# Performance work log

Measured on AMD Instinct MI355X. Metric: run time of the kernel, lower is better.

## Reference

```python
import jax, jax.numpy as jnp
import numpy as np

N, E, DIM_H, H = 50000, 400000, 128, 8
D = DIM_H // H  # 16


def _ln(x, g, b, eps=1e-5):
    mu = jnp.mean(x, axis=-1, keepdims=True)
    var = jnp.var(x, axis=-1, keepdims=True)
    return (x - mu) * jax.lax.rsqrt(var + eps) * g + b


def setup_inputs() -> dict:
    key = jax.random.key(0)
    ks = jax.random.split(key, 20)
    s = 1.0 / np.sqrt(DIM_H)
    lin = lambda k, i, o: jax.random.uniform(k, (i, o), jnp.float32, -s, s)
    inp = {
        "node_feature": jax.random.normal(ks[0], (N, DIM_H), jnp.float32),
        "edge_feature": jax.random.normal(ks[1], (E, DIM_H), jnp.float32),
        "Wq": lin(ks[2], DIM_H, DIM_H), "bq": jnp.zeros((DIM_H,), jnp.float32),
        "Wk": lin(ks[3], DIM_H, DIM_H), "bk": jnp.zeros((DIM_H,), jnp.float32),
        "Wv": lin(ks[4], DIM_H, DIM_H), "bv": jnp.zeros((DIM_H,), jnp.float32),
        "We": lin(ks[5], DIM_H, DIM_H), "be": jnp.zeros((DIM_H,), jnp.float32),
        "Wg": lin(ks[6], DIM_H, DIM_H), "bg": jnp.zeros((DIM_H,), jnp.float32),
        "Wo": lin(ks[7], DIM_H, DIM_H), "bo": jnp.zeros((DIM_H,), jnp.float32),
        "Woe": lin(ks[8], DIM_H, DIM_H), "boe": jnp.zeros((DIM_H,), jnp.float32),
        "ln1_g": jnp.ones((DIM_H,), jnp.float32), "ln1_b": jnp.zeros((DIM_H,), jnp.float32),
        "ln1e_g": jnp.ones((DIM_H,), jnp.float32), "ln1e_b": jnp.zeros((DIM_H,), jnp.float32),
        "ln2_g": jnp.ones((DIM_H,), jnp.float32), "ln2_b": jnp.zeros((DIM_H,), jnp.float32),
        "W1": lin(ks[9], DIM_H, 2 * DIM_H), "b1": jnp.zeros((2 * DIM_H,), jnp.float32),
        "W2": lin(ks[10], 2 * DIM_H, DIM_H) / np.sqrt(2.0), "b2": jnp.zeros((DIM_H,), jnp.float32),
        "edge_index": jax.random.randint(ks[11], (2, E), 0, N, jnp.int32),
    }
    return inp


def reference(node_feature, edge_feature, Wq, bq, Wk, bk, Wv, bv, We, be, Wg, bg,
              Wo, bo, Woe, boe, ln1_g, ln1_b, ln1e_g, ln1e_b, ln2_g, ln2_b,
              W1, b1, W2, b2, edge_index):
    x_in, e_in = node_feature, edge_feature
    src, dst = edge_index[0], edge_index[1]
    n = x_in.shape[0]

    x = _ln(x_in, ln1_g, ln1_b)
    e = _ln(e_in, ln1e_g, ln1e_b)

    # node projections -> [N, H, D]
    q = (x @ Wq + bq).reshape(n, H, D)
    k = (x @ Wk + bk).reshape(n, H, D)
    v = (x @ Wv + bv).reshape(n, H, D)
    # edge projections -> [E, H, D]
    ea = (e @ We + be).reshape(-1, H, D)
    eg = (e @ Wg + bg).reshape(-1, H, D)

    # gather along edges: [E, H, D]
    edge_q = q[dst]
    edge_k = k[src]
    edge_v = v[src] * jax.nn.sigmoid(eg)

    s_elt = edge_q * edge_k + ea                      # [E, H, D] (also edge output)
    scores = jnp.clip(jnp.sum(s_elt, axis=-1) / np.sqrt(D), -5.0, 5.0)  # [E, H]

    # scatter-softmax over destination nodes, per head
    m = jax.ops.segment_max(scores, dst, num_segments=n)      # [N, H]
    ex = jnp.exp(scores - m[dst])                             # [E, H]
    ssum = jax.ops.segment_sum(ex, dst, num_segments=n)       # [N, H]
    alpha = ex / ssum[dst]                                    # [E, H]

    # scatter-add aggregation
    out = jax.ops.segment_sum(alpha[..., None] * edge_v, dst, num_segments=n)  # [N, H, D]
    out = out.reshape(n, H * D)

    x_out = x_in + out @ Wo + bo
    e_out = e_in + s_elt.reshape(-1, H * D) @ Woe + boe

    # FFN ('Single') with pre-norm + residual
    h = _ln(x_out, ln2_g, ln2_b)
    x_out = x_out + jax.nn.relu(h @ W1 + b1) @ W2 + b2
    return x_out, e_out
```

## Files before the change

kernel.cpp:

```cpp
#include <hip/hip_runtime.h>

#define NN 50000
#define NE 400000
#define CAP 64
#define PACKN (7*16384 + 32768 + 32768)
#define PACKB ((PACKN + 255)/256)

typedef unsigned int u32;
typedef unsigned short u16;
typedef __attribute__((ext_vector_type(8))) short short8;
typedef __attribute__((ext_vector_type(4))) float f32x4;
typedef __attribute__((ext_vector_type(4))) unsigned int u32x4;

union FragU { uint4 u; short8 s; };
union Chunk { uint4 v[4]; u32 d[16]; };

__device__ __forceinline__ float bflo(u32 w){ union{u32 i; float f;} v; v.i = w<<16; return v.f; }
__device__ __forceinline__ float bfhi(u32 w){ union{u32 i; float f;} v; v.i = w & 0xffff0000u; return v.f; }
__device__ __forceinline__ u32 packbf(float a, float b){
  union{float f;u32 i;} x, y; x.f=a; y.f=b;
  u32 xi = x.i + (((x.i>>16)&1u) + 0x7fffu);
  u32 yi = y.i + (((y.i>>16)&1u) + 0x7fffu);
  return (xi>>16) | (yi & 0xffff0000u);
}

#define BAR() do { \
  asm volatile("s_waitcnt lgkmcnt(0)" ::: "memory"); \
  __builtin_amdgcn_s_barrier(); \
  asm volatile("" ::: "memory"); \
} while(0)

__device__ __forceinline__ int swz64(int row, int cp){ return row*64 + (cp ^ ((row&7)<<2)); }

__device__ __forceinline__ void stage_ln(const float* __restrict__ src, long base, long nrows,
                                         const float* __restrict__ gam, const float* __restrict__ bet,
                                         u32* __restrict__ tile, int t)
{
  int row = t>>2, sub = t&3;
  bool valid = (base + row) < nrows;
  const float* p = src + (base+row)*128 + sub*32;
  float4 x[8];
  float s=0.f, s2=0.f;
  #pragma unroll
  for(int q=0;q<8;++q){
    x[q] = valid ? *(const float4*)(p + 4*q) : make_float4(0.f,0.f,0.f,0.f);
    s  += x[q].x + x[q].y + x[q].z + x[q].w;
    s2 += x[q].x*x[q].x + x[q].y*x[q].y + x[q].z*x[q].z + x[q].w*x[q].w;
  }
  s  += __shfl_xor(s,1);  s  += __shfl_xor(s,2);
  s2 += __shfl_xor(s2,1); s2 += __shfl_xor(s2,2);
  float mu  = s*(1.f/128.f);
  float var = fmaxf(s2*(1.f/128.f) - mu*mu, 0.f);
  float rs  = rsqrtf(var + 1e-5f);
  const float* gp = gam + sub*32; const float* bp = bet + sub*32;
  #pragma unroll
  for(int m4=0;m4<4;++m4){
    float4 g0 = *(const float4*)(gp + 8*m4);
    float4 g1 = *(const float4*)(gp + 8*m4 + 4);
    float4 b0 = *(const float4*)(bp + 8*m4);
    float4 b1 = *(const float4*)(bp + 8*m4 + 4);
    float4 xa = x[2*m4], xb = x[2*m4+1];
    uint4 wv;
    wv.x = packbf((xa.x-mu)*rs*g0.x+b0.x, (xa.y-mu)*rs*g0.y+b0.y);
    wv.y = packbf((xa.z-mu)*rs*g0.z+b0.z, (xa.w-mu)*rs*g0.w+b0.w);
    wv.z = packbf((xb.x-mu)*rs*g1.x+b1.x, (xb.y-mu)*rs*g1.y+b1.y);
    wv.w = packbf((xb.z-mu)*rs*g1.z+b1.z, (xb.w-mu)*rs*g1.w+b1.w);
    *(uint4*)&tile[swz64(row, sub*16 + m4*4)] = wv;
  }
}

__device__ __forceinline__ void stage_ln8(const float* __restrict__ src, long base,
                                          const float* __restrict__ gam, const float* __restrict__ bet,
                                          u32* __restrict__ tile, int t)
{
  int row = t>>3, sub = t&7;
  const float* p = src + (base+row)*128 + sub*16;
  float4 x[4];
  float s=0.f, s2=0.f;
  #pragma unroll
  for(int q=0;q<4;++q){
    x[q] = *(const float4*)(p + 4*q);
    s  += x[q].x + x[q].y + x[q].z + x[q].w;
    s2 += x[q].x*x[q].x + x[q].y*x[q].y + x[q].z*x[q].z + x[q].w*x[q].w;
  }
  s  += __shfl_xor(s,1);  s  += __shfl_xor(s,2);  s  += __shfl_xor(s,4);
  s2 += __shfl_xor(s2,1); s2 += __shfl_xor(s2,2); s2 += __shfl_xor(s2,4);
  float mu  = s*(1.f/128.f);
  float var = fmaxf(s2*(1.f/128.f) - mu*mu, 0.f);
  float rs  = rsqrtf(var + 1e-5f);
  const float* gp = gam + sub*16; const float* bp = bet + sub*16;
  #pragma unroll
  for(int m4=0;m4<2;++m4){
    float4 g0 = *(const float4*)(gp + 8*m4);
    float4 g1 = *(const float4*)(gp + 8*m4 + 4);
    float4 b0 = *(const float4*)(bp + 8*m4);
    float4 b1 = *(const float4*)(bp + 8*m4 + 4);
    float4 xa = x[2*m4], xb = x[2*m4+1];
    uint4 wv;
    wv.x = packbf((xa.x-mu)*rs*g0.x+b0.x, (xa.y-mu)*rs*g0.y+b0.y);
    wv.y = packbf((xa.z-mu)*rs*g0.z+b0.z, (xa.w-mu)*rs*g0.w+b0.w);
    wv.z = packbf((xb.x-mu)*rs*g1.x+b1.x, (xb.y-mu)*rs*g1.y+b1.y);
    wv.w = packbf((xb.z-mu)*rs*g1.z+b1.z, (xb.w-mu)*rs*g1.w+b1.w);
    *(uint4*)&tile[swz64(row, sub*8 + m4*4)] = wv;
  }
}

__device__ __forceinline__ void gemmT8(const u16* __restrict__ PW, int NT, int mtoff,
                                       const u32* __restrict__ tile, int row, int l,
                                       f32x4 acc[8])
{
  int g = l>>4;
  #pragma unroll
  for(int kc=0;kc<4;++kc){
    FragU bf; bf.u = *(const uint4*)&tile[swz64(row, kc*16 + g*4)];
    #pragma unroll
    for(int mt=0;mt<8;++mt){
      FragU af; af.u = ((const uint4*)PW)[(size_t)(kc*NT + mtoff + mt)*64 + l];
      acc[mt] = __builtin_amdgcn_mfma_f32_16x16x32_bf16(af.s, bf.s, acc[mt], 0,0,0);
    }
  }
}

__device__ __forceinline__ void gemmT4(const u16* __restrict__ PW, int NT, int mtoff,
                                       const u32* __restrict__ tile, int row, int l,
                                       f32x4 acc[4])
{
  int g = l>>4;
  #pragma unroll
  for(int kc=0;kc<4;++kc){
    FragU bf; bf.u = *(const uint4*)&tile[swz64(row, kc*16 + g*4)];
    #pragma unroll
    for(int m=0;m<4;++m){
      FragU af; af.u = ((const uint4*)PW)[(size_t)(kc*NT + mtoff + m)*64 + l];
      acc[m] = __builtin_amdgcn_mfma_f32_16x16x32_bf16(af.s, bf.s, acc[m], 0,0,0);
    }
  }
}

__global__ __launch_bounds__(256)
void k_prep(const float* __restrict__ Wq, const float* __restrict__ Wk,
            const float* __restrict__ Wv, const float* __restrict__ We,
            const float* __restrict__ Wg, const float* __restrict__ Woe,
            const float* __restrict__ Wo, const float* __restrict__ W1,
            const float* __restrict__ W2, u16* __restrict__ dst,
            const int* __restrict__ eidx, int* __restrict__ cnt, int* __restrict__ elist)
{
  if (blockIdx.x < PACKB){
    int i = blockIdx.x*256 + threadIdx.x;
    const float* src; int N, idx;
    if (i < 7*16384){
      int m = i >> 14; idx = i & 16383; N=128;
      src = (m==0)?Wq:(m==1)?Wk:(m==2)?Wv:(m==3)?We:(m==4)?Wg:(m==5)?Woe:Wo;
    } else if (i < 7*16384 + 32768){ idx = i - 7*16384; N=256; src = W1; }
    else if (i < PACKN){ idx = i - 7*16384 - 32768; N=128; src = W2; }
    else return;
    int j = idx & 7, l = (idx>>3) & 63;
    int rest = idx >> 9;
    int NT = N >> 4;
    int nt = rest % NT, kc = rest / NT;
    int k = kc*32 + (l>>4)*8 + j;
    int n = nt*16 + (l&15);
    union{float f;u32 u;} x; x.f = src[(size_t)k*N + n];
    dst[i] = (u16)((x.u + (((x.u>>16)&1u) + 0x7fffu)) >> 16);
  } else {
    int e = (blockIdx.x - PACKB)*256 + threadIdx.x;
    if (e < NE){
      int d = eidx[NE+e];
      int pos = atomicAdd(&cnt[d], 1);
      if (pos < CAP) elist[(size_t)d*CAP + pos] = e;
    }
  }
}

__global__ __launch_bounds__(256)
void k_qkv(const float* __restrict__ xin,
           const float* __restrict__ l1g, const float* __restrict__ l1b,
           const u16* __restrict__ pWq, const float* __restrict__ bq,
           const u16* __restrict__ pWk, const float* __restrict__ bk,
           const u16* __restrict__ pWv, const float* __restrict__ bv,
           u32* __restrict__ qv, u32* __restrict__ kv, u32* __restrict__ vv)
{
  __shared__ u32 tile[64*64];
  int t = threadIdx.x;
  long base = (long)blockIdx.x * 64;
  stage_ln(xin, base, NN, l1g, l1b, tile, t);
  BAR();
  int w = t>>6, l = t&63, g = l>>4;
  int row = w*16 + (l&15);
  long node = base + row;
  bool valid = node < NN;

  f32x4 acc[8];
  const u16* pws[3] = {pWq, pWk, pWv};
  const float* bbs[3] = {bq, bk, bv};
  u32* outs[3] = {qv, kv, vv};
  #pragma unroll
  for(int s3=0;s3<3;++s3){
    #pragma unroll
    for(int mt=0;mt<8;++mt) acc[mt] = (f32x4){0.f,0.f,0.f,0.f};
    gemmT8(pws[s3], 8, 0, tile, row, l, acc);
    if (valid){
      Chunk c;
      #pragma unroll
      for(int mt=0;mt<8;++mt){
        float4 bb = *(const float4*)(bbs[s3] + mt*16 + g*4);
        c.d[mt*2]   = packbf(acc[mt][0]+bb.x, acc[mt][1]+bb.y);
        c.d[mt*2+1] = packbf(acc[mt][2]+bb.z, acc[mt][3]+bb.w);
      }
      uint4* op = (uint4*)(outs[s3] + node*64 + g*16);
      #pragma unroll
      for(int i=0;i<4;++i) op[i] = c.v[i];
    }
  }
}

__global__ __launch_bounds__(512)
void k_edge(const float* __restrict__ ein,
            const float* __restrict__ l1eg, const float* __restrict__ l1eb,
            const u16* __restrict__ pWg, const float* __restrict__ bg,
            const u16* __restrict__ pWe, const float* __restrict__ be,
            const u16* __restrict__ pWoe, const float* __restrict__ boe,
            const int* __restrict__ eidx,
            const u32* __restrict__ qv, const u32* __restrict__ kv, const u32* __restrict__ vv,
            u32* __restrict__ gvp, float* __restrict__ escp,
            float* __restrict__ eout)
{
  __shared__ u32 tile[64*64];
  int t = threadIdx.x;
  long base = (long)blockIdx.x * 64;
  stage_ln8(ein, base, l1eg, l1eb, tile, t);

  int w = t>>6, l = t&63, g = l>>4;
  int rg = w&3, half = w>>2;
  int row = rg*16 + (l&15);
  long edge = base + row;
  int s_ = eidx[edge], d_ = eidx[NE + edge];
  BAR();

  float4 er[4];
  #pragma unroll
  for(int m=0;m<4;++m)
    er[m] = *(const float4*)(ein + edge*128 + (half*4+m)*16 + g*4);

  const uint4* qp = (const uint4*)(qv + (size_t)d_*64 + g*16 + half*8);
  const uint4* kp = (const uint4*)(kv + (size_t)s_*64 + g*16 + half*8);
  uint4 qa = qp[0], qb = qp[1];
  uint4 ka = kp[0], kb = kp[1];
  uint2 qw[4] = {{qa.x,qa.y},{qa.z,qa.w},{qb.x,qb.y},{qb.z,qb.w}};
  uint2 kw[4] = {{ka.x,ka.y},{ka.z,ka.w},{kb.x,kb.y},{kb.z,kb.w}};

  f32x4 acc[4];
  #pragma unroll
  for(int m=0;m<4;++m) acc[m] = (f32x4){0.f,0.f,0.f,0.f};
  gemmT4(pWe, 8, half*4, tile, row, l, acc);
  float esc4[4];
  #pragma unroll
  for(int m=0;m<4;++m){
    int mt = half*4 + m;
    float4 bb = *(const float4*)(be + mt*16 + g*4);
    acc[m][0] += bb.x + bflo(qw[m].x)*bflo(kw[m].x);
    acc[m][1] += bb.y + bfhi(qw[m].x)*bfhi(kw[m].x);
    acc[m][2] += bb.z + bflo(qw[m].y)*bflo(kw[m].y);
    acc[m][3] += bb.w + bfhi(qw[m].y)*bfhi(kw[m].y);
    float ps = acc[m][0]+acc[m][1]+acc[m][2]+acc[m][3];
    ps += __shfl_xor(ps, 16);
    ps += __shfl_xor(ps, 32);
    float sc = fminf(fmaxf(ps*0.25f, -5.f), 5.f);
    esc4[m] = __expf(sc);
  }
  if (g==0){
    f32x4 e0 = {esc4[0],esc4[1],esc4[2],esc4[3]};
    __builtin_nontemporal_store(e0, (f32x4*)(escp + (size_t)edge*8 + half*4));
  }
  const uint4* vp = (const uint4*)(vv + (size_t)s_*64 + g*16 + half*8);
  uint4 va = vp[0], vb = vp[1];
  uint2 vw[4] = {{va.x,va.y},{va.z,va.w},{vb.x,vb.y},{vb.z,vb.w}};

  f32x4 gac[4];
  #pragma unroll
  for(int m=0;m<4;++m) gac[m] = (f32x4){0.f,0.f,0.f,0.f};
  gemmT4(pWg, 8, half*4, tile, row, l, gac);
  {
    u32 gd[8];
    #pragma unroll
    for(int m=0;m<4;++m){
      int mt = half*4 + m;
      float4 bb = *(const float4*)(bg + mt*16 + g*4);
      float g0 = 1.f/(1.f+__expf(-(gac[m][0]+bb.x)));
      float g1 = 1.f/(1.f+__expf(-(gac[m][1]+bb.y)));
      float g2 = 1.f/(1.f+__expf(-(gac[m][2]+bb.z)));
      float g3 = 1.f/(1.f+__expf(-(gac[m][3]+bb.w)));
      gd[m*2]   = packbf(g0*bflo(vw[m].x), g1*bfhi(vw[m].x));
      gd[m*2+1] = packbf(g2*bflo(vw[m].y), g3*bfhi(vw[m].y));
    }
    u32x4* gp = (u32x4*)(gvp + (size_t)edge*64 + g*16 + half*8);
    u32x4 g0 = {gd[0],gd[1],gd[2],gd[3]};
    u32x4 g1 = {gd[4],gd[5],gd[6],gd[7]};
    __builtin_nontemporal_store(g0, gp);
    __builtin_nontemporal_store(g1, gp+1);
  }
  BAR();
  #pragma unroll
  for(int m=0;m<4;++m){
    int mt = half*4 + m;
    uint2 o;
    o.x = packbf(acc[m][0], acc[m][1]);
    o.y = packbf(acc[m][2], acc[m][3]);
    *(uint2*)&tile[swz64(row, mt*8 + g*2)] = o;
  }
  BAR();
  f32x4 oac[4];
  #pragma unroll
  for(int m=0;m<4;++m) oac[m] = (f32x4){0.f,0.f,0.f,0.f};
  gemmT4(pWoe, 8, half*4, tile, row, l, oac);
  #pragma unroll
  for(int m=0;m<4;++m){
    int mt = half*4 + m;
    float4 bb = *(const float4*)(boe + mt*16 + g*4);
    f32x4 o;
    o[0] = er[m].x + oac[m][0] + bb.x;
    o[1] = er[m].y + oac[m][1] + bb.y;
    o[2] = er[m].z + oac[m][2] + bb.z;
    o[3] = er[m].w + oac[m][3] + bb.w;
    __builtin_nontemporal_store(o, (f32x4*)(eout + edge*128 + mt*16 + g*4));
  }
}

__global__ __launch_bounds__(256)
void k_agg(const u32* __restrict__ gvp, const float* __restrict__ escp,
           const int* __restrict__ elist, const int* __restrict__ cnt,
           u32* __restrict__ xattnb)
{
  int w = threadIdx.x>>6, l = threadIdx.x&63;
  long n = (long)blockIdx.x*4 + w;
  if (n >= NN) return;
  int h = (l&15)>>1;
  int e = min(cnt[n], CAP);
  const int* el = elist + (size_t)n*CAP;
  float s0=0.f, s1=0.f, den=0.f;
  int i = 0;
  for (; i+8<=e; i+=8){
    int ed[8];
    #pragma unroll
    for(int j=0;j<8;++j) ed[j] = el[i+j];
    u32 gw[8]; float a[8];
    #pragma unroll
    for(int j=0;j<8;++j){ gw[j] = gvp[(size_t)ed[j]*64 + l]; a[j] = escp[(size_t)ed[j]*8 + h]; }
    #pragma unroll
    for(int j=0;j<8;++j){ s0 += a[j]*bflo(gw[j]); s1 += a[j]*bfhi(gw[j]); den += a[j]; }
  }
  if (i < e){
    int m = e - i;
    int ed[7]; u32 gw[7]; float a[7];
    #pragma unroll
    for(int j=0;j<7;++j) if (j < m) ed[j] = el[i+j];
    #pragma unroll
    for(int j=0;j<7;++j) if (j < m){ gw[j] = gvp[(size_t)ed[j]*64 + l]; a[j] = escp[(size_t)ed[j]*8 + h]; }
    #pragma unroll
    for(int j=0;j<7;++j) if (j < m){ s0 += a[j]*bflo(gw[j]); s1 += a[j]*bfhi(gw[j]); den += a[j]; }
  }
  float inv = den>0.f ? 1.f/den : 0.f;
  xattnb[n*64 + l] = packbf(s0*inv, s1*inv);
}

__global__ __launch_bounds__(256)
void k_out(const float* __restrict__ xin,
           const u32* __restrict__ xattnb,
           const u16* __restrict__ pWo, const float* __restrict__ bo,
           const float* __restrict__ l2g, const float* __restrict__ l2b,
           const u16* __restrict__ pW1, const float* __restrict__ b1p,
           const u16* __restrict__ pW2, const float* __restrict__ b2p,
           float* __restrict__ xout)
{
  __shared__ u32 tile[64*64];
  __shared__ u32 hhalf[64*64];
  int t = threadIdx.x;
  long base = (long)blockIdx.x * 64;
  {
    int row = t>>2, sub = t&3;
    long node = base + row;
    bool valid = node < NN;
    Chunk c;
    if (valid){
      const uint4* p = (const uint4*)(xattnb + node*64 + sub*16);
      #pragma unroll
      for(int i=0;i<4;++i) c.v[i] = p[i];
    } else {
      #pragma unroll
      for(int i=0;i<16;++i) c.d[i] = 0;
    }
    #pragma unroll
    for(int mt=0;mt<8;++mt){
      uint2 o; o.x = c.d[mt*2]; o.y = c.d[mt*2+1];
      *(uint2*)&tile[swz64(row, mt*8 + sub*2)] = o;
    }
  }
  BAR();
  int w = t>>6, l = t&63, g = l>>4;
  int row = w*16 + (l&15);
  long node = base + row;
  bool valid = node < NN;

  float4 xr[8];
  #pragma unroll
  for(int mt=0;mt<8;++mt)
    xr[mt] = valid ? *(const float4*)(xin + node*128 + mt*16 + g*4) : make_float4(0.f,0.f,0.f,0.f);

  f32x4 acc[8], xm[8];
  #pragma unroll
  for(int mt=0;mt<8;++mt) acc[mt] = (f32x4){0.f,0.f,0.f,0.f};
  gemmT8(pWo, 8, 0, tile, row, l, acc);
  #pragma unroll
  for(int mt=0;mt<8;++mt){
    float4 bb = *(const float4*)(bo + mt*16 + g*4);
    xm[mt][0] = xr[mt].x + acc[mt][0] + bb.x;
    xm[mt][1] = xr[mt].y + acc[mt][1] + bb.y;
    xm[mt][2] = xr[mt].z + acc[mt][2] + bb.z;
    xm[mt][3] = xr[mt].w + acc[mt][3] + bb.w;
  }
  float s=0.f, s2=0.f;
  #pragma unroll
  for(int mt=0;mt<8;++mt){
    s  += xm[mt][0]+xm[mt][1]+xm[mt][2]+xm[mt][3];
    s2 += xm[mt][0]*xm[mt][0]+xm[mt][1]*xm[mt][1]+xm[mt][2]*xm[mt][2]+xm[mt][3]*xm[mt][3];
  }
  s  += __shfl_xor(s,16);  s  += __shfl_xor(s,32);
  s2 += __shfl_xor(s2,16); s2 += __shfl_xor(s2,32);
  float mu  = s*(1.f/128.f);
  float var = fmaxf(s2*(1.f/128.f) - mu*mu, 0.f);
  float rs  = rsqrtf(var + 1e-5f);
  BAR();
  #pragma unroll
  for(int mt=0;mt<8;++mt){
    float4 gg = *(const float4*)(l2g + mt*16 + g*4);
    float4 bb = *(const float4*)(l2b + mt*16 + g*4);
    float h0 = (xm[mt][0]-mu)*rs*gg.x + bb.x;
    float h1 = (xm[mt][1]-mu)*rs*gg.y + bb.y;
    float h2 = (xm[mt][2]-mu)*rs*gg.z + bb.z;
    float h3 = (xm[mt][3]-mu)*rs*gg.w + bb.w;
    uint2 o; o.x = packbf(h0,h1); o.y = packbf(h2,h3);
    *(uint2*)&tile[swz64(row, mt*8 + g*2)] = o;
  }
  BAR();
  f32x4 oacc[8];
  #pragma unroll
  for(int mt=0;mt<8;++mt) oacc[mt] = (f32x4){0.f,0.f,0.f,0.f};
  #pragma unroll
  for(int hf=0; hf<2; ++hf){
    f32x4 dh[8];
    #pragma unroll
    for(int mt=0;mt<8;++mt) dh[mt] = (f32x4){0.f,0.f,0.f,0.f};
    gemmT8(pW1, 16, hf*8, tile, row, l, dh);
    #pragma unroll
    for(int mt=0;mt<8;++mt){
      int feat = hf*128 + mt*16 + g*4;
      float4 bb = *(const float4*)(b1p + feat);
      float h0 = fmaxf(dh[mt][0]+bb.x, 0.f);
      float h1 = fmaxf(dh[mt][1]+bb.y, 0.f);
      float h2 = fmaxf(dh[mt][2]+bb.z, 0.f);
      float h3 = fmaxf(dh[mt][3]+bb.w, 0.f);
      uint2 o; o.x = packbf(h0,h1); o.y = packbf(h2,h3);
      *(uint2*)&hhalf[swz64(row, mt*8 + g*2)] = o;
    }
    BAR();
    gemmT8(pW2 + (size_t)hf*16384, 8, 0, hhalf, row, l, oacc);
    BAR();
  }
  if (valid){
    #pragma unroll
    for(int mt=0;mt<8;++mt){
      float4 bb = *(const float4*)(b2p + mt*16 + g*4);
      f32x4 o;
      o[0] = xm[mt][0] + oacc[mt][0] + bb.x;
      o[1] = xm[mt][1] + oacc[mt][1] + bb.y;
      o[2] = xm[mt][2] + oacc[mt][2] + bb.z;
      o[3] = xm[mt][3] + oacc[mt][3] + bb.w;
      __builtin_nontemporal_store(o, (f32x4*)(xout + node*128 + mt*16 + g*4));
    }
  }
}

extern "C" void kernel_launch(void* const* d_in, const int* in_sizes, int n_in,
                              void* d_out, int out_size, void* d_ws, size_t ws_size,
                              hipStream_t stream) {
  (void)in_sizes; (void)n_in; (void)out_size; (void)ws_size;
  const float* xin = (const float*)d_in[0];
  const float* ein = (const float*)d_in[1];
  const float* Wq = (const float*)d_in[2];  const float* bq = (const float*)d_in[3];
  const float* Wk = (const float*)d_in[4];  const float* bk = (const float*)d_in[5];
  const float* Wv = (const float*)d_in[6];  const float* bv = (const float*)d_in[7];
  const float* We = (const float*)d_in[8];  const float* be = (const float*)d_in[9];
  const float* Wg = (const float*)d_in[10]; const float* bg = (const float*)d_in[11];
  const float* Wo = (const float*)d_in[12]; const float* bo = (const float*)d_in[13];
  const float* Woe= (const float*)d_in[14]; const float* boe= (const float*)d_in[15];
  const float* l1g= (const float*)d_in[16]; const float* l1b= (const float*)d_in[17];
  const float* l1eg=(const float*)d_in[18]; const float* l1eb=(const float*)d_in[19];
  const float* l2g= (const float*)d_in[20]; const float* l2b= (const float*)d_in[21];
  const float* W1 = (const float*)d_in[22]; const float* b1 = (const float*)d_in[23];
  const float* W2 = (const float*)d_in[24]; const float* b2 = (const float*)d_in[25];
  const int* eidx = (const int*)d_in[26];

  float* xout = (float*)d_out;
  float* eout = xout + (size_t)NN*128;

  float* escp = (float*)d_ws;
  u32* gvp = (u32*)(escp + (size_t)NE*8);
  u32* qv = gvp + (size_t)NE*64;
  u32* kv = qv + (size_t)NN*64;
  u32* vv = kv + (size_t)NN*64;
  u32* xattnb = vv + (size_t)NN*64;
  int* cnt = (int*)(xattnb + (size_t)NN*64);
  int* elist = cnt + NN;
  u16* pw  = (u16*)(elist + (size_t)NN*CAP);
  u16* pWq = pw;            u16* pWk = pWq + 16384;  u16* pWv = pWk + 16384;
  u16* pWe = pWv + 16384;   u16* pWg = pWe + 16384;  u16* pWoe= pWg + 16384;
  u16* pWo = pWoe + 16384;  u16* pW1 = pWo + 16384;  u16* pW2 = pW1 + 32768;

  hipMemsetAsync(cnt, 0, NN*sizeof(int), stream);
  k_prep<<<PACKB + (NE+255)/256, 256, 0, stream>>>(Wq,Wk,Wv,We,Wg,Woe,Wo,W1,W2, pw,
                                                   eidx, cnt, elist);

  k_qkv<<<(NN+63)/64, 256, 0, stream>>>(xin, l1g, l1b, pWq, bq, pWk, bk, pWv, bv, qv, kv, vv);
  k_edge<<<NE/64, 512, 0, stream>>>(ein, l1eg, l1eb, pWg, bg, pWe, be, pWoe, boe,
                                    eidx, qv, kv, vv, gvp, escp, eout);
  k_agg<<<(NN+3)/4, 256, 0, stream>>>(gvp, escp, elist, cnt, xattnb);
  k_out<<<(NN+63)/64, 256, 0, stream>>>(xin, xattnb, pWo, bo, l2g, l2b,
                                        pW1, b1, pW2, b2, xout);
}
```

Baseline: 421.5 us.

## Fuse We and Wg edge GEMMs into one interleaved packed weight pass

Packs an interleaved We/Wg weight matrix in k_prep so the edge kernel runs one 8-tile GEMM over the LDS tile instead of two separate 4-tile GEMMs, and hoists the V gather load earlier. The gated-value output layout changes, so k_agg's head index mapping and k_out's tile scatter are adjusted to match. This is meant to cut repeated A-fragment LDS reads and loop overhead, at the cost of more live accumulator registers in a 512-thread kernel. The escp store also switches from nontemporal to a plain store.

```diff
diff --git a/kernel.cpp b/kernel.cpp
--- a/kernel.cpp
+++ b/kernel.cpp
@@ -4,7 +4,8 @@
 #define NE 400000
 #define CAP 64
 #define PACKN (7*16384 + 32768 + 32768)
-#define PACKB ((PACKN + 255)/256)
+#define PACKN2 (PACKN + 32768)
+#define PACKB ((PACKN2 + 255)/256)
 
 typedef unsigned int u32;
 typedef unsigned short u16;
@@ -147,17 +148,26 @@
 {
   if (blockIdx.x < PACKB){
     int i = blockIdx.x*256 + threadIdx.x;
-    const float* src; int N, idx;
+    const float* src; int N, idx, nt_override = -1;
     if (i < 7*16384){
       int m = i >> 14; idx = i & 16383; N=128;
       src = (m==0)?Wq:(m==1)?Wk:(m==2)?Wv:(m==3)?We:(m==4)?Wg:(m==5)?Woe:Wo;
     } else if (i < 7*16384 + 32768){ idx = i - 7*16384; N=256; src = W1; }
     else if (i < PACKN){ idx = i - 7*16384 - 32768; N=128; src = W2; }
+    else if (i < PACKN2){
+      idx = i - PACKN; N=128;
+      int rest = idx >> 9;
+      int T = rest & 15;
+      int half = T>>3, within = T&7;
+      nt_override = half*4 + (within&3);
+      src = (within>>2) ? Wg : We;
+    }
     else return;
     int j = idx & 7, l = (idx>>3) & 63;
     int rest = idx >> 9;
-    int NT = N >> 4;
-    int nt = rest % NT, kc = rest / NT;
+    int NT = (nt_override >= 0) ? 16 : (N >> 4);
+    int nt = (nt_override >= 0) ? nt_override : (rest % NT);
+    int kc = rest / NT;
     int k = kc*32 + (l>>4)*8 + j;
     int n = nt*16 + (l&15);
     union{float f;u32 u;} x; x.f = src[(size_t)k*N + n];
@@ -217,8 +227,8 @@
 __global__ __launch_bounds__(512)
 void k_edge(const float* __restrict__ ein,
             const float* __restrict__ l1eg, const float* __restrict__ l1eb,
-            const u16* __restrict__ pWg, const float* __restrict__ bg,
-            const u16* __restrict__ pWe, const float* __restrict__ be,
+            const u16* __restrict__ pWeg, const float* __restrict__ bg,
+            const float* __restrict__ be,
             const u16* __restrict__ pWoe, const float* __restrict__ boe,
             const int* __restrict__ eidx,
             const u32* __restrict__ qv, const u32* __restrict__ kv, const u32* __restrict__ vv,
@@ -241,71 +251,66 @@
   #pragma unroll
   for(int m=0;m<4;++m)
     er[m] = *(const float4*)(ein + edge*128 + (half*4+m)*16 + g*4);
-
   const uint4* qp = (const uint4*)(qv + (size_t)d_*64 + g*16 + half*8);
   const uint4* kp = (const uint4*)(kv + (size_t)s_*64 + g*16 + half*8);
+  const uint4* vp = (const uint4*)(vv + (size_t)s_*64 + g*16 + half*8);
   uint4 qa = qp[0], qb = qp[1];
   uint4 ka = kp[0], kb = kp[1];
+  uint4 va = vp[0], vb = vp[1];
   uint2 qw[4] = {{qa.x,qa.y},{qa.z,qa.w},{qb.x,qb.y},{qb.z,qb.w}};
   uint2 kw[4] = {{ka.x,ka.y},{ka.z,ka.w},{kb.x,kb.y},{kb.z,kb.w}};
-
-  f32x4 acc[4];
-  #pragma unroll
-  for(int m=0;m<4;++m) acc[m] = (f32x4){0.f,0.f,0.f,0.f};
-  gemmT4(pWe, 8, half*4, tile, row, l, acc);
+  uint2 vw[4] = {{va.x,va.y},{va.z,va.w},{vb.x,vb.y},{vb.z,vb.w}};
+
+  f32x4 acc8[8];
+  #pragma unroll
+  for(int m=0;m<8;++m) acc8[m] = (f32x4){0.f,0.f,0.f,0.f};
+  gemmT8(pWeg, 16, half*8, tile, row, l, acc8);
+
   float esc4[4];
   #pragma unroll
   for(int m=0;m<4;++m){
     int mt = half*4 + m;
     float4 bb = *(const float4*)(be + mt*16 + g*4);
-    acc[m][0] += bb.x + bflo(qw[m].x)*bflo(kw[m].x);
-    acc[m][1] += bb.y + bfhi(qw[m].x)*bfhi(kw[m].x);
-    acc[m][2] += bb.z + bflo(qw[m].y)*bflo(kw[m].y);
-    acc[m][3] += bb.w + bfhi(qw[m].y)*bfhi(kw[m].y);
-    float ps = acc[m][0]+acc[m][1]+acc[m][2]+acc[m][3];
+    acc8[m][0] += bb.x + bflo(qw[m].x)*bflo(kw[m].x);
+    acc8[m][1] += bb.y + bfhi(qw[m].x)*bfhi(kw[m].x);
+    acc8[m][2] += bb.z + bflo(qw[m].y)*bflo(kw[m].y);
+    acc8[m][3] += bb.w + bfhi(qw[m].y)*bfhi(kw[m].y);
+    float ps = acc8[m][0]+acc8[m][1]+acc8[m][2]+acc8[m][3];
     ps += __shfl_xor(ps, 16);
     ps += __shfl_xor(ps, 32);
     float sc = fminf(fmaxf(ps*0.25f, -5.f), 5.f);
     esc4[m] = __expf(sc);
   }
   if (g==0){
-    f32x4 e0 = {esc4[0],esc4[1],esc4[2],esc4[3]};
-    __builtin_nontemporal_store(e0, (f32x4*)(escp + (size_t)edge*8 + half*4));
-  }
-  const uint4* vp = (const uint4*)(vv + (size_t)s_*64 + g*16 + half*8);
-  uint4 va = vp[0], vb = vp[1];
-  uint2 vw[4] = {{va.x,va.y},{va.z,va.w},{vb.x,vb.y},{vb.z,vb.w}};
-
-  f32x4 gac[4];
-  #pragma unroll
-  for(int m=0;m<4;++m) gac[m] = (f32x4){0.f,0.f,0.f,0.f};
-  gemmT4(pWg, 8, half*4, tile, row, l, gac);
+    float4 e0 = {esc4[0],esc4[1],esc4[2],esc4[3]};
+    *(float4*)(escp + (size_t)edge*8 + half*4) = e0;
+  }
   {
     u32 gd[8];
     #pragma unroll
     for(int m=0;m<4;++m){
       int mt = half*4 + m;
       float4 bb = *(const float4*)(bg + mt*16 + g*4);
-      float g0 = 1.f/(1.f+__expf(-(gac[m][0]+bb.x)));
-      float g1 = 1.f/(1.f+__expf(-(gac[m][1]+bb.y)));
-      float g2 = 1.f/(1.f+__expf(-(gac[m][2]+bb.z)));
-      float g3 = 1.f/(1.f+__expf(-(gac[m][3]+bb.w)));
+      float g0 = 1.f/(1.f+__expf(-(acc8[4+m][0]+bb.x)));
+      float g1 = 1.f/(1.f+__expf(-(acc8[4+m][1]+bb.y)));
+      float g2 = 1.f/(1.f+__expf(-(acc8[4+m][2]+bb.z)));
+      float g3 = 1.f/(1.f+__expf(-(acc8[4+m][3]+bb.w)));
       gd[m*2]   = packbf(g0*bflo(vw[m].x), g1*bfhi(vw[m].x));
       gd[m*2+1] = packbf(g2*bflo(vw[m].y), g3*bfhi(vw[m].y));
     }
-    u32x4* gp = (u32x4*)(gvp + (size_t)edge*64 + g*16 + half*8);
-    u32x4 g0 = {gd[0],gd[1],gd[2],gd[3]};
-    u32x4 g1 = {gd[4],gd[5],gd[6],gd[7]};
-    __builtin_nontemporal_store(g0, gp);
-    __builtin_nontemporal_store(g1, gp+1);
+    u32x4* gp2 = (u32x4*)(gvp + (size_t)edge*64 + half*32 + g*8);
+    u32x4 g0v = {gd[0],gd[1],gd[2],gd[3]};
+    u32x4 g1v = {gd[4],gd[5],gd[6],gd[7]};
+    __builtin_nontemporal_store(g0v, gp2);
+    __builtin_nontemporal_store(g1v, gp2+1);
   }
   BAR();
   #pragma unroll
   for(int m=0;m<4;++m){
     int mt = half*4 + m;
     uint2 o;
-    o.x = packbf(acc[m][0], acc[m][1]);
-    o.y = packbf(acc[m][2], acc[m][3]);
+    o.x = packbf(acc8[m][0], acc8[m][1]);
+    o.y = packbf(acc8[m][2], acc8[m][3]);
     *(uint2*)&tile[swz64(row, mt*8 + g*2)] = o;
   }
   BAR();
@@ -334,7 +339,7 @@
   int w = threadIdx.x>>6, l = threadIdx.x&63;
   long n = (long)blockIdx.x*4 + w;
   if (n >= NN) return;
-  int h = (l&15)>>1;
+  int h = ((l>>5)<<2) | ((l>>1)&3);
   int e = min(cnt[n], CAP);
   const int* el = elist + (size_t)n*CAP;
   float s0=0.f, s1=0.f, den=0.f;
@@ -389,10 +394,14 @@
       #pragma unroll
       for(int i=0;i<16;++i) c.d[i] = 0;
     }
-    #pragma unroll
-    for(int mt=0;mt<8;++mt){
-      uint2 o; o.x = c.d[mt*2]; o.y = c.d[mt*2+1];
-      *(uint2*)&tile[swz64(row, mt*8 + sub*2)] = o;
+    int half = sub>>1;
+    #pragma unroll
+    for(int p=0;p<8;++p){
+      int g = (sub&1)*2 + (p>>2);
+      int m = p&3;
+      int cp = (half*4 + m)*8 + g*2;
+      uint2 o; o.x = c.d[2*p]; o.y = c.d[2*p+1];
+      *(uint2*)&tile[swz64(row, cp)] = o;
     }
   }
   BAR();
@@ -515,13 +524,15 @@
   u16* pWq = pw;            u16* pWk = pWq + 16384;  u16* pWv = pWk + 16384;
   u16* pWe = pWv + 16384;   u16* pWg = pWe + 16384;  u16* pWoe= pWg + 16384;
   u16* pWo = pWoe + 16384;  u16* pW1 = pWo + 16384;  u16* pW2 = pW1 + 32768;
+  u16* pWeg = pW2 + 32768;
+  (void)pWe; (void)pWg;
 
   hipMemsetAsync(cnt, 0, NN*sizeof(int), stream);
   k_prep<<<PACKB + (NE+255)/256, 256, 0, stream>>>(Wq,Wk,Wv,We,Wg,Woe,Wo,W1,W2, pw,
                                                    eidx, cnt, elist);
 
   k_qkv<<<(NN+63)/64, 256, 0, stream>>>(xin, l1g, l1b, pWq, bq, pWk, bk, pWv, bv, qv, kv, vv);
-  k_edge<<<NE/64, 512, 0, stream>>>(ein, l1eg, l1eb, pWg, bg, pWe, be, pWoe, boe,
+  k_edge<<<NE/64, 512, 0, stream>>>(ein, l1eg, l1eb, pWeg, bg, be, pWoe, boe,
                                     eidx, qv, kv, vv, gvp, escp, eout);
   k_agg<<<(NN+3)/4, 256, 0, stream>>>(gvp, escp, elist, cnt, xattnb);
   k_out<<<(NN+63)/64, 256, 0, stream>>>(xin, xattnb, pWo, bo, l2g, l2b,
```

Result: no change. 415.8 us (-1.3%).
